# Performance work log

Hardware: AMD Instinct MI355X
Metric: run time of the kernel (lower is better)

Reference implementation:

```python
import jax, jax.numpy as jnp
import numpy as np

B, T = 32, 2048            # batch, seq_len
V = 16                     # vocab_size
H = 256                    # hidden_size
NV = V + 2                 # embedding rows (padding_idx=0 + vocab + delimiter)
NO = V + 1                 # head output size


def setup_inputs() -> dict:
    key = jax.random.key(0)
    ks = jax.random.split(key, 8)
    s = 1.0 / np.sqrt(H).astype(np.float32)
    tokens = jax.random.randint(ks[0], (B, T), 0, NV)
    embed = jax.random.normal(ks[1], (NV, H), jnp.float32) * 0.02
    embed = embed.at[0].set(0.0)  # padding_idx=0
    # GRU params (PyTorch layout: gates [r|z|n] stacked on last dim)
    W_ih = jax.random.uniform(ks[2], (H, 3 * H), jnp.float32, -s, s)
    W_hh = jax.random.uniform(ks[3], (H, 3 * H), jnp.float32, -s, s)
    b_ih = jax.random.uniform(ks[4], (3 * H,), jnp.float32, -s, s)
    b_hh = jax.random.uniform(ks[5], (3 * H,), jnp.float32, -s, s)
    W_head = jax.random.uniform(ks[6], (H, NO), jnp.float32, -s, s)
    b_head = jax.random.uniform(ks[7], (NO,), jnp.float32, -s, s)
    return {"tokens": tokens, "embed": embed, "W_ih": W_ih, "W_hh": W_hh,
            "b_ih": b_ih, "b_hh": b_hh, "W_head": W_head, "b_head": b_head}


def _mogru_scan(x, W_ih, W_hh, b_ih, b_hh):
    # x: [B, T, H]. Precompute all input projections in one big GEMM.
    gi = x @ W_ih + b_ih                      # [B, T, 3H]
    gi_t = jnp.swapaxes(gi, 0, 1)             # [T, B, 3H] for scan
    h0 = jnp.zeros((x.shape[0], W_hh.shape[0]), x.dtype)

    def step(h, gi_step):
        gh = h @ W_hh + b_hh                  # [B, 3H]
        i_r, i_z, i_n = jnp.split(gi_step, 3, axis=-1)
        h_r, h_z, h_n = jnp.split(gh, 3, axis=-1)
        r = jax.nn.sigmoid(i_r + h_r)
        z = jax.nn.sigmoid(i_z + h_z)         # beta: retention gate
        n = jnp.tanh(i_n + r * h_n)
        h_new = (1.0 - z) * n + z * h
        return h_new, (h_new, z)

    h_last, (outs, betas) = jax.lax.scan(step, h0, gi_t)
    return jnp.swapaxes(outs, 0, 1), h_last, jnp.swapaxes(betas, 0, 1)


def reference(tokens, embed, W_ih, W_hh, b_ih, b_hh, W_head, b_head):
    x = embed[tokens]                          # [B, T, H] embedding lookup
    output, _, betas = _mogru_scan(x, W_ih, W_hh, b_ih, b_hh)
    logits = output @ W_head + b_head          # [B, T, V+1]
    return logits, betas
```

## Files before the change

### kernel.cpp

```cpp
#include <hip/hip_runtime.h>

#define BB   32
#define TT   2048
#define HH   256
#define G3   768
#define NVOC 18
#define NOUT 17
#define LOGITS_ELEMS ((size_t)BB * TT * NOUT)

typedef _Float16 h2 __attribute__((ext_vector_type(2)));

__device__ __forceinline__ float bf1(unsigned short u){
  union{unsigned int i; float f;} v; v.i = ((unsigned int)u) << 16; return v.f;
}
__device__ __forceinline__ unsigned short f2bf(float f){
  union{float f; unsigned int i;} v; v.f = f;
  unsigned int lsb = (v.i >> 16) & 1u;
  v.i += 0x7fffu + lsb;
  return (unsigned short)(v.i >> 16);
}
__device__ __forceinline__ float bflo(unsigned int u){
  union{unsigned int i; float f;} v; v.i = u << 16; return v.f;
}
__device__ __forceinline__ float bfhi(unsigned int u){
  union{unsigned int i; float f;} v; v.i = u & 0xffff0000u; return v.f;
}

__device__ __forceinline__ float ld1(const float* p, size_t i){ return p[i]; }
__device__ __forceinline__ float ld1(const unsigned short* p, size_t i){ return bf1(p[i]); }

__device__ __forceinline__ bool detect_f32(const void* W_ih_raw){
  const unsigned short* u = (const unsigned short*)W_ih_raw;
  bool big = false;
  #pragma unroll
  for (int i = 0; i < 64; i++){
    float v = bf1(u[i]);
    big |= !(v >= -0.25f && v <= 0.25f);
  }
  return big;
}

#if __has_builtin(__builtin_amdgcn_fdot2)
#define FDOT2(a,b,c) __builtin_amdgcn_fdot2((a),(b),(c),false)
#else
#define FDOT2(a,b,c) ((c) + (float)(a).x*(float)(b).x + (float)(a).y*(float)(b).y)
#endif

template<typename T>
__device__ __forceinline__ void proj_body(const T* embed, const T* W_ih,
                                          const T* b_ih, float* proj){
  int gid = blockIdx.x * 256 + threadIdx.x;
  if (gid >= NVOC * G3) return;
  int v = gid / G3;
  int j = gid - v * G3;
  float acc = ld1(b_ih, j);
  #pragma unroll 8
  for (int k = 0; k < HH; k++)
    acc += ld1(embed, (size_t)v * HH + k) * ld1(W_ih, (size_t)k * G3 + j);
  proj[gid] = acc;
}

__global__ __launch_bounds__(256) void k_proj(
    const void* __restrict__ embed, const void* __restrict__ W_ih,
    const void* __restrict__ b_ih, float* __restrict__ proj)
{
  if (detect_f32(W_ih))
    proj_body<float>((const float*)embed, (const float*)W_ih,
                     (const float*)b_ih, proj);
  else
    proj_body<unsigned short>((const unsigned short*)embed,
                              (const unsigned short*)W_ih,
                              (const unsigned short*)b_ih, proj);
}

template<typename T>
__device__ __forceinline__ void cache_cols(const T* W_hh, const T* b_hh,
                                           int j, h2* w, float& bhh){
  #pragma unroll
  for (int k = 0; k < 128; k++){
    float a0 = ld1(W_hh, (size_t)(2*k)   * G3 + j);
    float a1 = ld1(W_hh, (size_t)(2*k+1) * G3 + j);
    h2 t; t.x = (_Float16)a0; t.y = (_Float16)a1;
    w[k] = t;
  }
  bhh = ld1(b_hh, j);
}

__global__ __launch_bounds__(768, 1) void k_scan(
    const int*  __restrict__ tokens,
    const void* __restrict__ W_hh,
    const void* __restrict__ b_hh,
    const void* __restrict__ W_ih,
    const float* __restrict__ proj,
    unsigned short* __restrict__ outs,
    void* __restrict__ d_out_base)
{
  __shared__ float s_proj[NVOC * G3];
  __shared__ __align__(16) h2 s_h[HH / 2];
  __shared__ float s_z[HH];
  __shared__ float s_n[HH];

  const bool f32m = detect_f32(W_ih);
  const int b = blockIdx.x;
  const int j = threadIdx.x;

  for (int i = j; i < NVOC * G3; i += 768) s_proj[i] = proj[i];

  h2 w[128]; float bhh;
  if (f32m) cache_cols<float>((const float*)W_hh, (const float*)b_hh, j, w, bhh);
  else      cache_cols<unsigned short>((const unsigned short*)W_hh,
                                       (const unsigned short*)b_hh, j, w, bhh);

  if (j < HH/2) { h2 z; z.x = (_Float16)0.f; z.y = (_Float16)0.f; s_h[j] = z; }
  float h_old = 0.f;

  const int* tptr = tokens + (size_t)b * TT;
  int tok = tptr[0];
  const size_t base = (size_t)b * TT * HH + j;
  unsigned short* orow   = outs + base;
  unsigned short* brow_b = (unsigned short*)d_out_base + LOGITS_ELEMS + base;
  float*          brow_f = (float*)d_out_base          + LOGITS_ELEMS + base;

  __syncthreads();

  for (int t = 0; t < TT; t++) {
    int tok_next = (t + 1 < TT) ? tptr[t + 1] : 0;
    const float* pj = s_proj + tok * G3;
    float gi = pj[j];

    float a0 = 0.f, a1 = 0.f, a2 = 0.f, a3 = 0.f;
    const int4* hp = (const int4*)s_h;
    #pragma unroll
    for (int kk = 0; kk < 32; kk++) {
      int4 hv = hp[kk];
      a0 = FDOT2(w[4*kk+0], __builtin_bit_cast(h2, hv.x), a0);
      a1 = FDOT2(w[4*kk+1], __builtin_bit_cast(h2, hv.y), a1);
      a2 = FDOT2(w[4*kk+2], __builtin_bit_cast(h2, hv.z), a2);
      a3 = FDOT2(w[4*kk+3], __builtin_bit_cast(h2, hv.w), a3);
    }
    float gh = (a0 + a1) + (a2 + a3) + bhh;

    float r = 0.f;
    if (j >= 2*HH) {
      s_n[j - 2*HH] = gh;
    } else if (j >= HH) {
      s_z[j - HH] = 1.f / (1.f + __expf(-(gi + gh)));
    } else {
      r = 1.f / (1.f + __expf(-(gi + gh)));
    }
    __syncthreads();

    if (j < HH) {
      float z = s_z[j];
      float x = pj[2*HH + j] + r * s_n[j];
      x = fminf(fmaxf(x, -15.f), 15.f);
      float e = __expf(2.f * x);
      float n = (e - 1.f) / (e + 1.f);
      float hn = (1.f - z) * n + z * h_old;
      h_old = hn;
      ((_Float16*)s_h)[j] = (_Float16)hn;
      orow[(size_t)t * HH] = f2bf(hn);
      if (f32m) brow_f[(size_t)t * HH] = z;
      else      brow_b[(size_t)t * HH] = f2bf(z);
    }
    __syncthreads();
    tok = tok_next;
  }
}

template<typename T>
__device__ __forceinline__ void stage_head(const T* W_head, const T* b_head,
                                           float* s_w, float* s_b, int tid){
  for (int i = tid; i < NOUT * HH; i += 256) {
    int o = i / HH, k = i - o * HH;
    s_w[i] = ld1(W_head, (size_t)k * NOUT + o);
  }
  if (tid < NOUT) s_b[tid] = ld1(b_head, (size_t)tid);
}

__global__ __launch_bounds__(256) void k_head(
    const unsigned short* __restrict__ outs,
    const void* __restrict__ W_head,
    const void* __restrict__ b_head,
    const void* __restrict__ W_ih,
    void* __restrict__ logits_out)
{
  __shared__ float s_w[NOUT * HH];
  __shared__ float s_b[NOUT];
  const bool f32m = detect_f32(W_ih);
  const int tid = threadIdx.x;

  if (f32m) stage_head<float>((const float*)W_head, (const float*)b_head,
                              s_w, s_b, tid);
  else      stage_head<unsigned short>((const unsigned short*)W_head,
                                       (const unsigned short*)b_head,
                                       s_w, s_b, tid);
  __syncthreads();

  size_t gid = (size_t)blockIdx.x * 256 + tid;
  if (gid >= LOGITS_ELEMS) return;
  int o = (int)(gid % NOUT);
  size_t row = gid / NOUT;

  const uint4* xp = (const uint4*)(outs + row * HH);
  const float* wv = s_w + o * HH;
  float a0 = 0.f, a1 = 0.f, a2 = 0.f, a3 = 0.f;
  #pragma unroll 8
  for (int kk = 0; kk < 32; kk++) {
    uint4 u = xp[kk];
    int kb = kk * 8;
    a0 += bflo(u.x) * wv[kb+0] + bfhi(u.x) * wv[kb+1];
    a1 += bflo(u.y) * wv[kb+2] + bfhi(u.y) * wv[kb+3];
    a2 += bflo(u.z) * wv[kb+4] + bfhi(u.z) * wv[kb+5];
    a3 += bflo(u.w) * wv[kb+6] + bfhi(u.w) * wv[kb+7];
  }
  float val = ((a0 + a1) + (a2 + a3)) + s_b[o];
  if (f32m) ((float*)logits_out)[gid] = val;
  else      ((unsigned short*)logits_out)[gid] = f2bf(val);
}

extern "C" void kernel_launch(void* const* d_in, const int* in_sizes, int n_in,
                              void* d_out, int out_size, void* d_ws, size_t ws_size,
                              hipStream_t stream)
{
  const int* tokens = (const int*)d_in[0];
  const void* embed  = d_in[1];
  const void* W_ih   = d_in[2];
  const void* W_hh   = d_in[3];
  const void* b_ih   = d_in[4];
  const void* b_hh   = d_in[5];
  const void* W_head = d_in[6];
  const void* b_head = d_in[7];

  float*          proj = (float*)d_ws;
  unsigned short* outs = (unsigned short*)((char*)d_ws + (size_t)NVOC * G3 * 4);

  k_proj<<<(NVOC * G3 + 255) / 256, 256, 0, stream>>>(embed, W_ih, b_ih, proj);
  k_scan<<<BB, 768, 0, stream>>>(tokens, W_hh, b_hh, W_ih, proj, outs, d_out);
  k_head<<<(int)((LOGITS_ELEMS + 255) / 256), 256, 0, stream>>>(
      outs, W_head, b_head, W_ih, d_out);
}
```

Baseline: 2.866 ms.

## Split recurrent dot product across thread pairs with prepacked fp16 weights

```diff
diff --git a/kernel.cpp b/kernel.cpp
--- a/kernel.cpp
+++ b/kernel.cpp
@@ -47,53 +47,62 @@
 #endif
 
 template<typename T>
+__device__ __forceinline__ void prep_body(const T* W_hh, _Float16* Wp){
+  int j = blockIdx.x;
+  int e = threadIdx.x;
+  int q = j & 1, p = j >> 1;
+  int c = e >> 7, i = e & 127;
+  float v = ld1(W_hh, (size_t)(128*q + i) * G3 + 2*p + c);
+  Wp[(size_t)j * 256 + e] = (_Float16)v;
+}
+
+__global__ __launch_bounds__(256) void k_prep(
+    const void* __restrict__ W_hh, const void* __restrict__ W_ih,
+    _Float16* __restrict__ Wp)
+{
+  if (detect_f32(W_ih)) prep_body<float>((const float*)W_hh, Wp);
+  else                  prep_body<unsigned short>((const unsigned short*)W_hh, Wp);
+}
+
+template<typename T>
 __device__ __forceinline__ void proj_body(const T* embed, const T* W_ih,
-                                          const T* b_ih, float* proj){
-  int gid = blockIdx.x * 256 + threadIdx.x;
-  if (gid >= NVOC * G3) return;
-  int v = gid / G3;
-  int j = gid - v * G3;
-  float acc = ld1(b_ih, j);
+                                          const T* b_ih, const T* b_hh,
+                                          float* proj, float* bb){
+  __shared__ float s_e[HH];
+  int v = blockIdx.x, j = threadIdx.x;
+  if (j < HH) s_e[j] = ld1(embed, (size_t)v * HH + j);
+  if (v == 0) bb[j] = ld1(b_hh, (size_t)j);
+  __syncthreads();
+  float acc = ld1(b_ih, (size_t)j);
   #pragma unroll 8
   for (int k = 0; k < HH; k++)
-    acc += ld1(embed, (size_t)v * HH + k) * ld1(W_ih, (size_t)k * G3 + j);
-  proj[gid] = acc;
-}
-
-__global__ __launch_bounds__(256) void k_proj(
+    acc += s_e[k] * ld1(W_ih, (size_t)k * G3 + j);
+  proj[(size_t)v * G3 + j] = acc;
+}
+
+__global__ __launch_bounds__(768) void k_proj(
     const void* __restrict__ embed, const void* __restrict__ W_ih,
-    const void* __restrict__ b_ih, float* __restrict__ proj)
+    const void* __restrict__ b_ih, const void* __restrict__ b_hh,
+    float* __restrict__ proj, float* __restrict__ bb)
 {
   if (detect_f32(W_ih))
     proj_body<float>((const float*)embed, (const float*)W_ih,
-                     (const float*)b_ih, proj);
+                     (const float*)b_ih, (const float*)b_hh, proj, bb);
   else
     proj_body<unsigned short>((const unsigned short*)embed,
                               (const unsigned short*)W_ih,
-                              (const unsigned short*)b_ih, proj);
-}
-
-template<typename T>
-__device__ __forceinline__ void cache_cols(const T* W_hh, const T* b_hh,
-                                           int j, h2* w, float& bhh){
-  #pragma unroll
-  for (int k = 0; k < 128; k++){
-    float a0 = ld1(W_hh, (size_t)(2*k)   * G3 + j);
-    float a1 = ld1(W_hh, (size_t)(2*k+1) * G3 + j);
-    h2 t; t.x = (_Float16)a0; t.y = (_Float16)a1;
-    w[k] = t;
-  }
-  bhh = ld1(b_hh, j);
+                              (const unsigned short*)b_ih,
+                              (const unsigned short*)b_hh, proj, bb);
 }
 
 __global__ __launch_bounds__(768, 1) void k_scan(
-    const int*  __restrict__ tokens,
-    const void* __restrict__ W_hh,
-    const void* __restrict__ b_hh,
-    const void* __restrict__ W_ih,
-    const float* __restrict__ proj,
+    const int*      __restrict__ tokens,
+    const _Float16* __restrict__ Wp,
+    const float*    __restrict__ bb,
+    const void*     __restrict__ W_ih,
+    const float*    __restrict__ proj,
     unsigned short* __restrict__ outs,
-    void* __restrict__ d_out_base)
+    void*           __restrict__ d_out_base)
 {
   __shared__ float s_proj[NVOC * G3];
   __shared__ __align__(16) h2 s_h[HH / 2];
@@ -103,48 +112,83 @@
   const bool f32m = detect_f32(W_ih);
   const int b = blockIdx.x;
   const int j = threadIdx.x;
+  const int q16 = (j & 1) * 16;
 
   for (int i = j; i < NVOC * G3; i += 768) s_proj[i] = proj[i];
 
-  h2 w[128]; float bhh;
-  if (f32m) cache_cols<float>((const float*)W_hh, (const float*)b_hh, j, w, bhh);
-  else      cache_cols<unsigned short>((const unsigned short*)W_hh,
-                                       (const unsigned short*)b_hh, j, w, bhh);
+  h2 wA[64], wB[64];
+  {
+    const float4* wp4 = (const float4*)(Wp + (size_t)j * 256);
+    #pragma unroll
+    for (int i = 0; i < 16; i++){
+      float4 v = wp4[i];
+      wA[4*i+0] = __builtin_bit_cast(h2, v.x);
+      wA[4*i+1] = __builtin_bit_cast(h2, v.y);
+      wA[4*i+2] = __builtin_bit_cast(h2, v.z);
+      wA[4*i+3] = __builtin_bit_cast(h2, v.w);
+    }
+    #pragma unroll
+    for (int i = 0; i < 16; i++){
+      float4 v = wp4[16 + i];
+      wB[4*i+0] = __builtin_bit_cast(h2, v.x);
+      wB[4*i+1] = __builtin_bit_cast(h2, v.y);
+      wB[4*i+2] = __builtin_bit_cast(h2, v.z);
+      wB[4*i+3] = __builtin_bit_cast(h2, v.w);
+    }
+  }
+  const float bhh = bb[j];
 
   if (j < HH/2) { h2 z; z.x = (_Float16)0.f; z.y = (_Float16)0.f; s_h[j] = z; }
   float h_old = 0.f;
 
   const int* tptr = tokens + (size_t)b * TT;
   int tok = tptr[0];
-  const size_t base = (size_t)b * TT * HH + j;
-  unsigned short* orow   = outs + base;
-  unsigned short* brow_b = (unsigned short*)d_out_base + LOGITS_ELEMS + base;
-  float*          brow_f = (float*)d_out_base          + LOGITS_ELEMS + base;
+  unsigned short* orow   = outs + (size_t)b * TT * HH + j;
+  unsigned short* brow_b = (unsigned short*)d_out_base + LOGITS_ELEMS
+                           + (size_t)b * TT * HH + (j - HH);
+  float*          brow_f = (float*)d_out_base + LOGITS_ELEMS
+                           + (size_t)b * TT * HH + (j - HH);
 
   __syncthreads();
 
   for (int t = 0; t < TT; t++) {
     int tok_next = (t + 1 < TT) ? tptr[t + 1] : 0;
     const float* pj = s_proj + tok * G3;
-    float gi = pj[j];
+    float gi  = pj[j];
+    float gin = (j < HH) ? pj[2*HH + j] : 0.f;
 
     float a0 = 0.f, a1 = 0.f, a2 = 0.f, a3 = 0.f;
     const int4* hp = (const int4*)s_h;
     #pragma unroll
-    for (int kk = 0; kk < 32; kk++) {
-      int4 hv = hp[kk];
-      a0 = FDOT2(w[4*kk+0], __builtin_bit_cast(h2, hv.x), a0);
-      a1 = FDOT2(w[4*kk+1], __builtin_bit_cast(h2, hv.y), a1);
-      a2 = FDOT2(w[4*kk+2], __builtin_bit_cast(h2, hv.z), a2);
-      a3 = FDOT2(w[4*kk+3], __builtin_bit_cast(h2, hv.w), a3);
-    }
-    float gh = (a0 + a1) + (a2 + a3) + bhh;
+    for (int i = 0; i < 16; i++) {
+      int4 hv = hp[q16 + i];
+      h2 x0 = __builtin_bit_cast(h2, hv.x);
+      h2 x1 = __builtin_bit_cast(h2, hv.y);
+      h2 x2 = __builtin_bit_cast(h2, hv.z);
+      h2 x3 = __builtin_bit_cast(h2, hv.w);
+      a0 = FDOT2(wA[4*i+0], x0, a0);
+      a1 = FDOT2(wA[4*i+1], x1, a1);
+      a0 = FDOT2(wA[4*i+2], x2, a0);
+      a1 = FDOT2(wA[4*i+3], x3, a1);
+      a2 = FDOT2(wB[4*i+0], x0, a2);
+      a3 = FDOT2(wB[4*i+1], x1, a3);
+      a2 = FDOT2(wB[4*i+2], x2, a2);
+      a3 = FDOT2(wB[4*i+3], x3, a3);
+    }
+    float accA = a0 + a1;
+    float accB = a2 + a3;
+    accA += __shfl_xor(accA, 1);
+    accB += __shfl_xor(accB, 1);
+    float gh = ((j & 1) ? accB : accA) + bhh;
 
     float r = 0.f;
     if (j >= 2*HH) {
       s_n[j - 2*HH] = gh;
     } else if (j >= HH) {
-      s_z[j - HH] = 1.f / (1.f + __expf(-(gi + gh)));
+      float z = 1.f / (1.f + __expf(-(gi + gh)));
+      s_z[j - HH] = z;
+      if (f32m) brow_f[(size_t)t * HH] = z;
+      else      brow_b[(size_t)t * HH] = f2bf(z);
     } else {
       r = 1.f / (1.f + __expf(-(gi + gh)));
     }
@@ -152,7 +196,7 @@
 
     if (j < HH) {
       float z = s_z[j];
-      float x = pj[2*HH + j] + r * s_n[j];
+      float x = gin + r * s_n[j];
       x = fminf(fmaxf(x, -15.f), 15.f);
       float e = __expf(2.f * x);
       float n = (e - 1.f) / (e + 1.f);
@@ -160,8 +204,6 @@
       h_old = hn;
       ((_Float16*)s_h)[j] = (_Float16)hn;
       orow[(size_t)t * HH] = f2bf(hn);
-      if (f32m) brow_f[(size_t)t * HH] = z;
-      else      brow_b[(size_t)t * HH] = f2bf(z);
     }
     __syncthreads();
     tok = tok_next;
@@ -232,11 +274,15 @@
   const void* W_head = d_in[6];
   const void* b_head = d_in[7];
 
-  float*          proj = (float*)d_ws;
-  unsigned short* outs = (unsigned short*)((char*)d_ws + (size_t)NVOC * G3 * 4);
-
-  k_proj<<<(NVOC * G3 + 255) / 256, 256, 0, stream>>>(embed, W_ih, b_ih, proj);
-  k_scan<<<BB, 768, 0, stream>>>(tokens, W_hh, b_hh, W_ih, proj, outs, d_out);
+  char* ws = (char*)d_ws;
+  float*          proj = (float*)ws;
+  float*          bb   = (float*)(ws + 55296);
+  _Float16*       Wp   = (_Float16*)(ws + 55296 + 3072);
+  unsigned short* outs = (unsigned short*)(ws + 55296 + 3072 + 393216);
+
+  k_prep<<<G3, 256, 0, stream>>>(W_hh, W_ih, Wp);
+  k_proj<<<NVOC, G3, 0, stream>>>(embed, W_ih, b_ih, b_hh, proj, bb);
+  k_scan<<<BB, G3, 0, stream>>>(tokens, Wp, bb, W_ih, proj, outs, d_out);
   k_head<<<(int)((LOGITS_ELEMS + 255) / 256), 256, 0, stream>>>(
       outs, W_head, b_head, W_ih, d_out);
 }
```

After: 2.718 ms. 5.2% less time.
